# Kernel tuning notes

Hardware: AMD Instinct MI355X
Metric: run time of the kernel (lower is better)

Reference implementation:

```python
import jax, jax.numpy as jnp
import numpy as np

N_CELL, N_DRUG = 8192, 4096


def setup_inputs() -> dict:
    key = jax.random.key(0)
    adj = jax.random.uniform(key, (N_CELL, N_DRUG), dtype=jnp.float32)
    return {"adj": adj}


def reference(adj):
    # Degree normalizations with +1 self-loop smoothing, as in the torch module.
    d_x = (jnp.sum(adj, axis=1) + 1.0) ** -0.5  # [N_CELL]
    d_y = (jnp.sum(adj, axis=0) + 1.0) ** -0.5  # [N_DRUG]

    # diag(d_x) @ adj @ diag(d_y) == row/col broadcast scaling (same math, O(n^2)).
    agg_cell_lp = d_x[:, None] * adj * d_y[None, :]          # [N_CELL, N_DRUG]
    agg_drug_lp = d_y[:, None] * adj.T * d_x[None, :]        # [N_DRUG, N_CELL]

    d_c = (jnp.sum(adj, axis=1) + 1.0) ** -1.0               # [N_CELL]
    self_cell_lp = jnp.diag(d_c + 1.0)                       # [N_CELL, N_CELL]
    d_d = (jnp.sum(adj, axis=0) + 1.0) ** -1.0               # [N_DRUG]
    self_drug_lp = jnp.diag(d_d + 1.0)                       # [N_DRUG, N_DRUG]

    return (agg_cell_lp, agg_drug_lp, self_cell_lp, self_drug_lp)
```

## Files before the change

### kernel.cpp

```cpp
#include <hip/hip_runtime.h>

#define N_CELL 8192
#define N_DRUG 4096

typedef float f32x4 __attribute__((ext_vector_type(4)));

static constexpr size_t OFF1 = (size_t)N_CELL * N_DRUG;
static constexpr size_t OFF2 = 2ull * N_CELL * N_DRUG;
static constexpr size_t OFF3 = OFF2 + (size_t)N_CELL * N_CELL;
static constexpr size_t FILL_F4 = ((size_t)N_CELL * N_CELL + (size_t)N_DRUG * N_DRUG) / 4;

#define SUM_BLOCKS 512
#define FILL_BLOCKS 1536
#define MEGA_BLOCKS (SUM_BLOCKS + FILL_BLOCKS)

__global__ __launch_bounds__(256) void mega_kernel(const float* __restrict__ adj,
                                                   float* __restrict__ rowsum,
                                                   float* __restrict__ colsum,
                                                   float* __restrict__ fill_base) {
    int b = blockIdx.x;
    int tid = threadIdx.x;
    if (b >= SUM_BLOCKS) {
        f32x4 z = {0.f, 0.f, 0.f, 0.f};
        f32x4* p = reinterpret_cast<f32x4*>(fill_base);
        for (size_t i = (size_t)(b - SUM_BLOCKS) * 256 + tid; i < FILL_F4;
             i += (size_t)FILL_BLOCKS * 256) {
            __builtin_nontemporal_store(z, p + i);
        }
        return;
    }
    __shared__ float lds_row[64][4];
    int cb = b & 3;
    int rb = b >> 2;
    int c0 = cb * 1024;
    int r0 = rb * 64;
    int lane = tid & 63, w = tid >> 6;
    const f32x4* ap = reinterpret_cast<const f32x4*>(adj + (size_t)r0 * N_DRUG + c0) + tid;
    f32x4 cacc = {0.f, 0.f, 0.f, 0.f};
#pragma unroll 4
    for (int r = 0; r < 64; ++r) {
        f32x4 v = ap[(size_t)r * (N_DRUG / 4)];
        cacc += v;
        float h = (v.x + v.y) + (v.z + v.w);
#pragma unroll
        for (int off = 32; off > 0; off >>= 1) h += __shfl_down(h, off, 64);
        if (lane == 0) lds_row[r][w] = h;
    }
    __syncthreads();
    if (tid < 64) {
        float s = (lds_row[tid][0] + lds_row[tid][1]) + (lds_row[tid][2] + lds_row[tid][3]);
        atomicAdd(&rowsum[r0 + tid], s);
    }
    int c = c0 + tid * 4;
    atomicAdd(&colsum[c + 0], cacc.x);
    atomicAdd(&colsum[c + 1], cacc.y);
    atomicAdd(&colsum[c + 2], cacc.z);
    atomicAdd(&colsum[c + 3], cacc.w);
}

__global__ __launch_bounds__(256) void scale_kernel(const float* __restrict__ adj,
                                                    const float* __restrict__ rowsum,
                                                    const float* __restrict__ colsum,
                                                    float* __restrict__ out) {
    __shared__ float tile[64][69];
    int tid = threadIdx.x;
    int tx = tid & 15;
    int ty = tid >> 4;
    int c0 = blockIdx.x * 64;
    int r0 = blockIdx.y * 64;

    if (blockIdx.y == 0) {
        int gid = blockIdx.x * 256 + tid;
        if (gid < N_CELL) {
            out[OFF2 + (size_t)gid * (N_CELL + 1)] = 1.0f / (rowsum[gid] + 1.0f) + 1.0f;
        } else if (gid < N_CELL + N_DRUG) {
            int j = gid - N_CELL;
            out[OFF3 + (size_t)j * (N_DRUG + 1)] = 1.0f / (colsum[j] + 1.0f) + 1.0f;
        }
    }

    f32x4 cs = *reinterpret_cast<const f32x4*>(colsum + c0 + tx * 4);
    f32x4 dy;
    dy.x = rsqrtf(cs.x + 1.0f);
    dy.y = rsqrtf(cs.y + 1.0f);
    dy.z = rsqrtf(cs.z + 1.0f);
    dy.w = rsqrtf(cs.w + 1.0f);

#pragma unroll
    for (int q = 0; q < 4; ++q) {
        int rr = q * 16 + ty;
        int r = r0 + rr;
        float dx = rsqrtf(rowsum[r] + 1.0f);
        f32x4 v = *reinterpret_cast<const f32x4*>(adj + (size_t)r * N_DRUG + c0 + tx * 4);
        f32x4 o = v * dx;
        o *= dy;
        __builtin_nontemporal_store(
            o, reinterpret_cast<f32x4*>(out + (size_t)r * N_DRUG + c0 + tx * 4));
        tile[rr][tx * 4 + 0] = o.x;
        tile[rr][tx * 4 + 1] = o.y;
        tile[rr][tx * 4 + 2] = o.z;
        tile[rr][tx * 4 + 3] = o.w;
    }
    __syncthreads();
    float* aggd = out + OFF1;
#pragma unroll
    for (int q = 0; q < 4; ++q) {
        int dr = q * 16 + ty;
        f32x4 o;
        o.x = tile[tx * 4 + 0][dr];
        o.y = tile[tx * 4 + 1][dr];
        o.z = tile[tx * 4 + 2][dr];
        o.w = tile[tx * 4 + 3][dr];
        __builtin_nontemporal_store(
            o, reinterpret_cast<f32x4*>(aggd + (size_t)(c0 + dr) * N_CELL + r0 + tx * 4));
    }
}

extern "C" void kernel_launch(void* const* d_in, const int* in_sizes, int n_in,
                              void* d_out, int out_size, void* d_ws, size_t ws_size,
                              hipStream_t stream) {
    const float* adj = (const float*)d_in[0];
    float* out = (float*)d_out;
    float* rowsum = (float*)d_ws;
    float* colsum = rowsum + N_CELL;

    (void)hipMemsetAsync(d_ws, 0, (N_CELL + N_DRUG) * sizeof(float), stream);

    mega_kernel<<<MEGA_BLOCKS, 256, 0, stream>>>(adj, rowsum, colsum, out + OFF2);
    scale_kernel<<<dim3(N_DRUG / 64, N_CELL / 64), 256, 0, stream>>>(adj, rowsum, colsum, out);
}
```

Baseline: 162.1 us.

## Split zero-fill into hipMemset, separate diag kernel, and shorten row-sum shuffle reduction

```diff
diff --git a/kernel.cpp b/kernel.cpp
--- a/kernel.cpp
+++ b/kernel.cpp
@@ -8,33 +8,16 @@
 static constexpr size_t OFF1 = (size_t)N_CELL * N_DRUG;
 static constexpr size_t OFF2 = 2ull * N_CELL * N_DRUG;
 static constexpr size_t OFF3 = OFF2 + (size_t)N_CELL * N_CELL;
-static constexpr size_t FILL_F4 = ((size_t)N_CELL * N_CELL + (size_t)N_DRUG * N_DRUG) / 4;
 
-#define SUM_BLOCKS 512
-#define FILL_BLOCKS 1536
-#define MEGA_BLOCKS (SUM_BLOCKS + FILL_BLOCKS)
-
-__global__ __launch_bounds__(256) void mega_kernel(const float* __restrict__ adj,
+__global__ __launch_bounds__(256) void sums_kernel(const float* __restrict__ adj,
                                                    float* __restrict__ rowsum,
-                                                   float* __restrict__ colsum,
-                                                   float* __restrict__ fill_base) {
-    int b = blockIdx.x;
+                                                   float* __restrict__ colsum) {
+    __shared__ float part[64][65];
     int tid = threadIdx.x;
-    if (b >= SUM_BLOCKS) {
-        f32x4 z = {0.f, 0.f, 0.f, 0.f};
-        f32x4* p = reinterpret_cast<f32x4*>(fill_base);
-        for (size_t i = (size_t)(b - SUM_BLOCKS) * 256 + tid; i < FILL_F4;
-             i += (size_t)FILL_BLOCKS * 256) {
-            __builtin_nontemporal_store(z, p + i);
-        }
-        return;
-    }
-    __shared__ float lds_row[64][4];
-    int cb = b & 3;
-    int rb = b >> 2;
+    int cb = blockIdx.x & 3;
+    int rb = blockIdx.x >> 2;
     int c0 = cb * 1024;
     int r0 = rb * 64;
-    int lane = tid & 63, w = tid >> 6;
     const f32x4* ap = reinterpret_cast<const f32x4*>(adj + (size_t)r0 * N_DRUG + c0) + tid;
     f32x4 cacc = {0.f, 0.f, 0.f, 0.f};
 #pragma unroll 4
@@ -42,13 +25,15 @@
         f32x4 v = ap[(size_t)r * (N_DRUG / 4)];
         cacc += v;
         float h = (v.x + v.y) + (v.z + v.w);
-#pragma unroll
-        for (int off = 32; off > 0; off >>= 1) h += __shfl_down(h, off, 64);
-        if (lane == 0) lds_row[r][w] = h;
+        h += __shfl_down(h, 1, 64);
+        h += __shfl_down(h, 2, 64);
+        if ((tid & 3) == 0) part[r][tid >> 2] = h;
     }
     __syncthreads();
     if (tid < 64) {
-        float s = (lds_row[tid][0] + lds_row[tid][1]) + (lds_row[tid][2] + lds_row[tid][3]);
+        float s = 0.f;
+#pragma unroll 8
+        for (int j = 0; j < 64; ++j) s += part[tid][j];
         atomicAdd(&rowsum[r0 + tid], s);
     }
     int c = c0 + tid * 4;
@@ -68,16 +53,6 @@
     int ty = tid >> 4;
     int c0 = blockIdx.x * 64;
     int r0 = blockIdx.y * 64;
-
-    if (blockIdx.y == 0) {
-        int gid = blockIdx.x * 256 + tid;
-        if (gid < N_CELL) {
-            out[OFF2 + (size_t)gid * (N_CELL + 1)] = 1.0f / (rowsum[gid] + 1.0f) + 1.0f;
-        } else if (gid < N_CELL + N_DRUG) {
-            int j = gid - N_CELL;
-            out[OFF3 + (size_t)j * (N_DRUG + 1)] = 1.0f / (colsum[j] + 1.0f) + 1.0f;
-        }
-    }
 
     f32x4 cs = *reinterpret_cast<const f32x4*>(colsum + c0 + tx * 4);
     f32x4 dy;
@@ -116,6 +91,18 @@
     }
 }
 
+__global__ __launch_bounds__(256) void diag_kernel(const float* __restrict__ rowsum,
+                                                   const float* __restrict__ colsum,
+                                                   float* __restrict__ out) {
+    int i = blockIdx.x * 256 + threadIdx.x;
+    if (i < N_CELL) {
+        out[OFF2 + (size_t)i * (N_CELL + 1)] = 1.0f / (rowsum[i] + 1.0f) + 1.0f;
+    } else if (i < N_CELL + N_DRUG) {
+        int j = i - N_CELL;
+        out[OFF3 + (size_t)j * (N_DRUG + 1)] = 1.0f / (colsum[j] + 1.0f) + 1.0f;
+    }
+}
+
 extern "C" void kernel_launch(void* const* d_in, const int* in_sizes, int n_in,
                               void* d_out, int out_size, void* d_ws, size_t ws_size,
                               hipStream_t stream) {
@@ -126,6 +113,12 @@
 
     (void)hipMemsetAsync(d_ws, 0, (N_CELL + N_DRUG) * sizeof(float), stream);
 
-    mega_kernel<<<MEGA_BLOCKS, 256, 0, stream>>>(adj, rowsum, colsum, out + OFF2);
+    sums_kernel<<<512, 256, 0, stream>>>(adj, rowsum, colsum);
     scale_kernel<<<dim3(N_DRUG / 64, N_CELL / 64), 256, 0, stream>>>(adj, rowsum, colsum, out);
+
+    (void)hipMemsetAsync(out + OFF2,
+                         0,
+                         ((size_t)N_CELL * N_CELL + (size_t)N_DRUG * N_DRUG) * sizeof(float),
+                         stream);
+    diag_kernel<<<48, 256, 0, stream>>>(rowsum, colsum, out);
 }
```

After: 176.4 us. 1.09x slower.
